# Optimization experiments

Hardware: AMD Instinct MI355X
Metric: run time of the kernel (lower is better)

## Reference

```python
import jax, jax.numpy as jnp
import numpy as np

B, G, D, E = 16, 2048, 2048, 32          # batch, genes, drug fp dim, gene embed dim
NL, NM, H, GS = 16, 4, 6, 64             # n leaves, n mids, term hidden, genes per leaf
GAMMA, NDRUG, EPS = 0.5, 1024, 1e-5

def _bn3(x):  # BatchNorm1d on [B, C, L], training stats, affine at init (gamma=1, beta=0)
    m = x.mean(axis=(0, 2), keepdims=True)
    v = x.var(axis=(0, 2), keepdims=True)
    return (x - m) / jnp.sqrt(v + EPS)

def _bn2(x):  # BatchNorm1d on [B, C]
    m = x.mean(axis=0, keepdims=True)
    v = x.var(axis=0, keepdims=True)
    return (x - m) / jnp.sqrt(v + EPS)

def _term(ci, W1, b1, Wc, bc, Wd, bd):
    # ci: [B, E, in] child input; returns ([B,H,E] 3d out, [B,H] 2d out)
    h = jnp.einsum('bei,hi->bhe', ci, W1) + b1[None, :, None]      # linear -> permute
    h = _bn3(h)
    c = jnp.einsum('bhe,kh->bke', h, Wc) + bc[None, :, None]       # context layer
    out3d = _bn3(c)                                                # [B,H,E]
    mean = out3d.mean(axis=1)                                      # [B,E]
    out2d = _bn2(jnp.tanh(mean @ Wd.T + bd))                       # dimension layer
    return out3d, out2d

def setup_inputs():
    key = jax.random.key(0)
    ks = iter(jax.random.split(key, 64))
    def rn(shape):
        return jax.random.normal(next(ks), shape, dtype=jnp.float32) * 0.05
    x = jax.random.normal(next(ks), (B, G + D + 1), dtype=jnp.float32)
    idx = jax.random.randint(next(ks), (B,), 0, NDRUG)
    x = x.at[:, -1].set(idx.astype(jnp.float32))
    table = jax.random.randint(next(ks), (NDRUG, G), 0, G, dtype=jnp.int32)
    inp = dict(x=x, table=table,
        W_rbf=rn((E, G)), b_rbf=rn((E,)), emb=rn((G, E)),
        W_dg=rn((NL, GS, G)), b_dg=rn((NL, GS)),
        Wl1=rn((NL, H, GS)), bl1=rn((NL, H)), Wlc=rn((NL, H, H)), blc=rn((NL, H)),
        Wld=rn((NL, H, E)), bld=rn((NL, H)),
        Wm1=rn((NM, H, 4 * H)), bm1=rn((NM, H)), Wmc=rn((NM, H, H)), bmc=rn((NM, H)),
        Wmd=rn((NM, H, E)), bmd=rn((NM, H)),
        Wr1=rn((H, 4 * H)), br1=rn((H,)), Wrc=rn((H, H)), brc=rn((H,)),
        Wrd=rn((H, E)), brd=rn((H,)),
        Wd1=rn((100, D)), bd1=rn((100,)), Wd2=rn((50, 100)), bd2=rn((50,)),
        Wd3=rn((H, 50)), bd3=rn((H,)),
        Wf=rn((6, 2 * H)), bf=rn((6,)), Wfa=rn((1, 6)), bfa=rn((1,)),
        Wfo=rn((1, 1)), bfo=rn((1,)))
    return inp

def reference(x, W_rbf, b_rbf, emb, W_dg, b_dg,
              Wl1, bl1, Wlc, blc, Wld, bld,
              Wm1, bm1, Wmc, bmc, Wmd, bmd,
              Wr1, br1, Wrc, brc, Wrd, brd,
              Wd1, bd1, Wd2, bd2, Wd3, bd3,
              Wf, bf, Wfa, bfa, Wfo, bfo, table):
    g = x[:, :G]
    drug = x[:, G:G + D]
    idx = x[:, G + D].astype(jnp.int32)
    # RBF kernel: [B, G, G]
    vect = jnp.exp(-GAMMA * jnp.square(g[:, :, None] - g[:, None, :]))
    gv = jnp.einsum('bij,ej->bie', vect, W_rbf) + b_rbf            # [B,G,E]
    lv = emb[table[idx]]                                            # [B,G,E]
    gf = (gv + lv).transpose(0, 2, 1)                               # [B,E,G]
    # per-leaf direct gene layers
    gene_out = jnp.einsum('beg,lkg->lbek', gf, W_dg) + b_dg[:, None, None, :]  # [NL,B,E,GS]
    leaf3d, _ = jax.vmap(_term)(gene_out, Wl1, bl1, Wlc, blc, Wld, bld)        # [NL,B,H,E]
    # mid terms: concat 4 leaf children along feature dim
    a = leaf3d.transpose(0, 1, 3, 2).reshape(NM, 4, B, E, H)
    a = jnp.moveaxis(a, 1, 3).reshape(NM, B, E, 4 * H)
    mid3d, _ = jax.vmap(_term)(a, Wm1, bm1, Wmc, bmc, Wmd, bmd)                # [NM,B,H,E]
    r = jnp.moveaxis(mid3d.transpose(0, 1, 3, 2), 0, 2).reshape(B, E, 4 * H)
    _, root2d = _term(r, Wr1, br1, Wrc, brc, Wrd, brd)                          # [B,H]
    # drug MLP
    d = drug
    for Wl, bl in ((Wd1, bd1), (Wd2, bd2), (Wd3, bd3)):
        d = _bn2(jnp.tanh(d @ Wl.T + bl))
    fin = jnp.concatenate([root2d, d], axis=1)                                  # [B,2H]
    out = _bn2(jnp.tanh(fin @ Wf.T + bf))
    aux = jnp.tanh(out @ Wfa.T + bfa)
    return aux @ Wfo.T + bfo                                                    # [B,1]
```

## Files before the change

### kernel.cpp

```cpp
#include <hip/hip_runtime.h>
#include <hip/hip_bf16.h>

#define Bb 16
#define Gg 2048
#define Dd 2048
#define XS 4097
#define EPSf 1e-5f
#define CEXP (-0.72134752044448170368f)

typedef unsigned int u32;
typedef __attribute__((ext_vector_type(8))) short bf16x8;
typedef __attribute__((ext_vector_type(4))) float f32x4;

union U16 { uint4 u; bf16x8 v; };

__device__ inline float fast_exp2(float x) {
#if __has_builtin(__builtin_amdgcn_exp2f)
  return __builtin_amdgcn_exp2f(x);
#else
  return exp2f(x);
#endif
}

__device__ inline u32 pk2(float a, float b) {
// ... 18 lines not shown
__device__ inline float wred(float v) {
  #pragma unroll
  for (int o = 32; o > 0; o >>= 1) v += __shfl_xor(v, o, 64);
  return v;
}

__global__ __launch_bounds__(256) void k_split(const float* __restrict__ Wrbf,
                                               const float* __restrict__ Wdg,
                                               u32* __restrict__ Rhi, u32* __restrict__ Rlo,
                                               u32* __restrict__ Dhi, u32* __restrict__ Dlo) {
  int c = blockIdx.x * 256 + threadIdx.x;
  const float* src;
  u32 *dhi, *dlo;
  if (c < 8192) {
    int h = c >> 12, ks = (c >> 6) & 63, l = c & 63;
    src = Wrbf + (h * 16 + (l & 15)) * Gg + ks * 32 + (l >> 4) * 8;
    dhi = Rhi + (size_t)c * 4; dlo = Rlo + (size_t)c * 4;
  } else {
    int cc = c - 8192;
    int nf = cc >> 12, ks = (cc >> 6) & 63, l = cc & 63;
    src = Wdg + (size_t)(nf * 16 + (l & 15)) * Gg + ks * 32 + (l >> 4) * 8;
    dhi = Dhi + (size_t)cc * 4; dlo = Dlo + (size_t)cc * 4;
  }
  float4 f0 = *(const float4*)src;
  float4 f1 = *(const float4*)(src + 4);
  float f[8] = {f0.x, f0.y, f0.z, f0.w, f1.x, f1.y, f1.z, f1.w};
  U16 hi, lo;
  split8(f, hi, lo);
  *(uint4*)dhi = hi.u;
  *(uint4*)dlo = lo.u;
}

__global__ __launch_bounds__(512) void k_rbf(const float* __restrict__ x,
                                             const u32* __restrict__ Whi,
                                             const u32* __restrict__ Wlo,
                                             const int* __restrict__ table,
                                             const float* __restrict__ emb,
                                             const float* __restrict__ brbf,
                                             u32* __restrict__ Ahi,
                                             u32* __restrict__ Alo) {
  __shared__ float g_s[2048];
  __shared__ u32 w_s[8192];
  const int tid = threadIdx.x;
  const int lane = tid & 63, wid = tid >> 6;
  const int b = blockIdx.y;
  const int i0w = blockIdx.x * 128 + wid * 16;
  #pragma unroll
  for (int q = 0; q < 4; ++q) g_s[tid * 4 + q] = x[(size_t)b * XS + tid * 4 + q];
  const float gi = x[(size_t)b * XS + i0w + (lane & 15)];
  f32x4 acc0 = {0.f, 0.f, 0.f, 0.f};
  f32x4 acc1 = {0.f, 0.f, 0.f, 0.f};
  const int jb = (lane >> 4) * 8;

  for (int chunk = 0; chunk < 8; ++chunk) {
    __syncthreads();
    #pragma unroll
    for (int sg = 0; sg < 4; ++sg) {
      int seg = wid * 4 + sg;
      int arr = seg >> 4, h = (seg >> 3) & 1, ksl = seg & 7;
      const u32* src = (arr ? Wlo : Whi) +
          (((size_t)h * 64 + chunk * 8 + ksl) * 64 + lane) * 4;
      *(uint4*)&w_s[seg * 256 + lane * 4] = *(const uint4*)src;
    }
    __syncthreads();
    #pragma unroll
    for (int ksl = 0; ksl < 8; ++ksl) {
      const float* gp = &g_s[chunk * 256 + ksl * 32 + jb];
      float4 gja = *(const float4*)gp;
      float4 gjb = *(const float4*)(gp + 4);
      float gv[8] = {gja.x, gja.y, gja.z, gja.w, gjb.x, gjb.y, gjb.z, gjb.w};
      float kv[8];
      #pragma unroll
      for (int q = 0; q < 8; ++q) {
        float d = gi - gv[q];
        kv[q] = fast_exp2(d * d * CEXP);
      }
      U16 ah, al;
      split8(kv, ah, al);
      U16 w0h, w1h, w0l, w1l;
      w0h.u = *(const uint4*)&w_s[(ksl) * 256 + lane * 4];
      w1h.u = *(const uint4*)&w_s[(8 + ksl) * 256 + lane * 4];
      w0l.u = *(const uint4*)&w_s[(16 + ksl) * 256 + lane * 4];
      w1l.u = *(const uint4*)&w_s[(24 + ksl) * 256 + lane * 4];
      acc0 = __builtin_amdgcn_mfma_f32_16x16x32_bf16(ah.v, w0h.v, acc0, 0, 0, 0);
      acc0 = __builtin_amdgcn_mfma_f32_16x16x32_bf16(al.v, w0h.v, acc0, 0, 0, 0);
      acc0 = __builtin_amdgcn_mfma_f32_16x16x32_bf16(ah.v, w0l.v, acc0, 0, 0, 0);
      acc1 = __builtin_amdgcn_mfma_f32_16x16x32_bf16(ah.v, w1h.v, acc1, 0, 0, 0);
      acc1 = __builtin_amdgcn_mfma_f32_16x16x32_bf16(al.v, w1h.v, acc1, 0, 0, 0);
      acc1 = __builtin_amdgcn_mfma_f32_16x16x32_bf16(ah.v, w1l.v, acc1, 0, 0, 0);
    }
  }
  const int idx = (int)x[(size_t)b * XS + Gg + Dd];
  const int eloc = lane & 15, quad = lane >> 4;
  const int ks = i0w >> 5;
  const int lp = (2 * ((i0w >> 4) & 1) + (quad >> 1)) * 16 + eloc;
  const int hs = quad & 1;
  #pragma unroll
  for (int hb = 0; hb < 2; ++hb) {
    const int e = hb * 16 + eloc;
    const float bias = brbf[e];
    f32x4 a = hb ? acc1 : acc0;
    float v[4];
    #pragma unroll
    for (int r = 0; r < 4; ++r) {
      int i = i0w + quad * 4 + r;
      int t = table[idx * Gg + i];
      v[r] = a[r] + bias + emb[t * 32 + e];
    }
    size_t off = ((size_t)((b * 2 + hb) * 64 + ks) * 64 + lp) * 4 + hs * 2;
    Ahi[off]     = pk2(v[0], v[1]);
    Ahi[off + 1] = pk2(v[2], v[3]);
    Alo[off]     = pk2(v[0] - bftrunc(v[0]), v[1] - bftrunc(v[1]));
    Alo[off + 1] = pk2(v[2] - bftrunc(v[2]), v[3] - bftrunc(v[3]));
  }
}

__global__ __launch_bounds__(256) void k_mm(const u32* __restrict__ Ahi,
                                            const u32* __restrict__ Alo,
                                            const u32* __restrict__ Bhi,
                                            const u32* __restrict__ Blo,
                                            float* __restrict__ part) {
  __shared__ u32 s_mm[6144];
  const int tid = threadIdx.x;
  const int lane = tid & 63, wid = tid >> 6;
  const int id = blockIdx.x;
  const int pl = id & 7, by = (id >> 3) & 7, ph = id >> 6;
  const int p = ph * 8 + pl;
  const int bx = p >> 2, kc = p & 3;
  const int wm = wid >> 1, wn = wid & 1;
  f32x4 acc[2][4];
  #pragma unroll
  for (int mf = 0; mf < 2; ++mf)
    #pragma unroll
    for (int nf = 0; nf < 4; ++nf) acc[mf][nf] = (f32x4){0.f, 0.f, 0.f, 0.f};

  for (int stage = 0; stage < 16; ++stage) {
    const int ks = kc * 16 + stage;
    __syncthreads();
    #pragma unroll
    for (int q = 0; q < 6; ++q) {
      int seg = wid * 6 + q;
      const u32* src;
      if (seg < 8) {
        int hl = seg >> 2, mf = seg & 3;
        src = (hl ? Alo : Ahi) + (((size_t)(by * 4 + mf) * 64 + ks) * 64 + lane) * 4;
      } else {
        int t = seg - 8, hl = t >> 3, nf = t & 7;
        src = (hl ? Blo : Bhi) + (((size_t)(bx * 8 + nf) * 64 + ks) * 64 + lane) * 4;
      }
      *(uint4*)&s_mm[seg * 256 + lane * 4] = *(const uint4*)src;
    }
    __syncthreads();
    U16 ah[2], al[2], bh[4], bl[4];
    #pragma unroll
    for (int mf = 0; mf < 2; ++mf) {
      ah[mf].u = *(const uint4*)&s_mm[(0 + wm * 2 + mf) * 256 + lane * 4];
      al[mf].u = *(const uint4*)&s_mm[(4 + wm * 2 + mf) * 256 + lane * 4];
    }
    #pragma unroll
    for (int nf = 0; nf < 4; ++nf) {
      bh[nf].u = *(const uint4*)&s_mm[(8 + wn * 4 + nf) * 256 + lane * 4];
      bl[nf].u = *(const uint4*)&s_mm[(16 + wn * 4 + nf) * 256 + lane * 4];
    }
    #pragma unroll
    for (int mf = 0; mf < 2; ++mf) {
      #pragma unroll
      for (int nf = 0; nf < 4; ++nf) {
        acc[mf][nf] = __builtin_amdgcn_mfma_f32_16x16x32_bf16(ah[mf].v, bh[nf].v, acc[mf][nf], 0, 0, 0);
        acc[mf][nf] = __builtin_amdgcn_mfma_f32_16x16x32_bf16(al[mf].v, bh[nf].v, acc[mf][nf], 0, 0, 0);
        acc[mf][nf] = __builtin_amdgcn_mfma_f32_16x16x32_bf16(ah[mf].v, bl[nf].v, acc[mf][nf], 0, 0, 0);
      }
    }
  }
  const int quad = lane >> 4, nl = lane & 15;
  #pragma unroll
  for (int mf = 0; mf < 2; ++mf) {
    #pragma unroll
    for (int nf = 0; nf < 4; ++nf) {
      int n  = bx * 128 + wn * 64 + nf * 16 + nl;
      int m0 = by * 64 + wm * 32 + mf * 16 + quad * 4;
      float4 st = make_float4(acc[mf][nf][0], acc[mf][nf][1], acc[mf][nf][2], acc[mf][nf][3]);
      *(float4*)&part[(size_t)kc * 524288 + (size_t)n * 512 + m0] = st;
    }
  }
}

__device__ inline void bn512(float* v, int wv, int lane,
                             float (*r1)[6], float (*r2)[6]) {
  float s[6], q[6];
  #pragma unroll
  for (int c = 0; c < 6; ++c) {
    float a = v[c];
    s[c] = wred(a);
    q[c] = wred(a * a);
  }
  __syncthreads();
  if (lane == 0) {
    #pragma unroll
    for (int c = 0; c < 6; ++c) { r1[wv][c] = s[c]; r2[wv][c] = q[c]; }
  }
  __syncthreads();
  #pragma unroll
  for (int c = 0; c < 6; ++c) {
    float S = 0.f, Q = 0.f;
    #pragma unroll
    for (int w = 0; w < 8; ++w) { S += r1[w][c]; Q += r2[w][c]; }
    float m  = S * (1.0f / 512.0f);
    float va = Q * (1.0f / 512.0f) - m * m;
    v[c] = (v[c] - m) * rsqrtf(va + EPSf);
  }
}

__global__ __launch_bounds__(512) void k_leaf(const float* __restrict__ part,
                                              const float* __restrict__ bdg,
                                              const float* __restrict__ W1,
                                              const float* __restrict__ b1,
                                              const float* __restrict__ Wc,
                                              const float* __restrict__ bc,
                                              float* __restrict__ outp) {
  const int l = blockIdx.x, tid = threadIdx.x;
  const int wv = tid >> 6, lane = tid & 63;
  __shared__ float r1[8][6], r2[8][6];
  float cv[64];
  #pragma unroll
  for (int i = 0; i < 64; ++i) {
    int n = l * 64 + i;
    const float* pp = part + (size_t)n * 512 + tid;
    cv[i] = pp[0] + pp[524288] + pp[2 * 524288] + pp[3 * 524288] + bdg[n];
  }
  const float* w1 = W1 + l * 6 * 64;
  float h[6];
  #pragma unroll
  for (int hh = 0; hh < 6; ++hh) {
    float s = b1[l * 6 + hh];
    #pragma unroll
    for (int i = 0; i < 64; ++i) s = fmaf(cv[i], w1[hh * 64 + i], s);
    h[hh] = s;
  }
  bn512(h, wv, lane, r1, r2);
  float c[6];
  #pragma unroll
  for (int k = 0; k < 6; ++k) {
    float s = bc[l * 6 + k];
    #pragma unroll
    for (int hh = 0; hh < 6; ++hh) s = fmaf(h[hh], Wc[l * 36 + k * 6 + hh], s);
    c[k] = s;
  }
  bn512(c, wv, lane, r1, r2);
  float* o = outp + (((size_t)(l >> 2) * 512 + tid) * 24 + (l & 3) * 6);
  #pragma unroll
  for (int k = 0; k < 6; ++k) o[k] = c[k];
}

__global__ __launch_bounds__(512) void k_mid(const float* __restrict__ gin,
                                             const float* __restrict__ W1,
                                             const float* __restrict__ b1,
                                             const float* __restrict__ Wc,
                                             const float* __restrict__ bc,
                                             float* __restrict__ outp) {
  const int l = blockIdx.x, tid = threadIdx.x;
  const int wv = tid >> 6, lane = tid & 63;
  __shared__ float r1[8][6], r2[8][6];
  const float* ci = gin + ((size_t)l * 512 + tid) * 24;
  float cv[24];
  #pragma unroll
  for (int q = 0; q < 6; ++q) *(float4*)&cv[q * 4] = ((const float4*)ci)[q];
  const float* w1 = W1 + l * 6 * 24;
  float h[6];
  #pragma unroll
  for (int hh = 0; hh < 6; ++hh) {
    float s = b1[l * 6 + hh];
    #pragma unroll
    for (int i = 0; i < 24; ++i) s = fmaf(cv[i], w1[hh * 24 + i], s);
    h[hh] = s;
  }
  bn512(h, wv, lane, r1, r2);
  float c[6];
  #pragma unroll
  for (int k = 0; k < 6; ++k) {
    float s = bc[l * 6 + k];
    #pragma unroll
    for (int hh = 0; hh < 6; ++hh) s = fmaf(h[hh], Wc[l * 36 + k * 6 + hh], s);
    c[k] = s;
  }
  bn512(c, wv, lane, r1, r2);
  float* o = outp + ((size_t)tid * 24 + l * 6);
  #pragma unroll
  for (int k = 0; k < 6; ++k) o[k] = c[k];
}

__global__ __launch_bounds__(512) void k_root(const float* __restrict__ rootin,
                                              const float* __restrict__ Wr1,
                                              const float* __restrict__ br1,
                                              const float* __restrict__ Wrc,
                                              const float* __restrict__ brc,
                                              const float* __restrict__ Wrd,
                                              const float* __restrict__ brd,
                                              float* __restrict__ r2d) {
  const int tid = threadIdx.x;
  const int wv = tid >> 6, lane = tid & 63;
  __shared__ float r1[8][6], r2[8][6];
  const float* ci = rootin + (size_t)tid * 24;
  float cv[24];
  #pragma unroll
  for (int q = 0; q < 6; ++q) *(float4*)&cv[q * 4] = ((const float4*)ci)[q];
  float h[6];
  #pragma unroll
  for (int hh = 0; hh < 6; ++hh) {
    float s = br1[hh];
    #pragma unroll
    for (int i = 0; i < 24; ++i) s = fmaf(cv[i], Wr1[hh * 24 + i], s);
    h[hh] = s;
  }
  bn512(h, wv, lane, r1, r2);
  float c[6];
  #pragma unroll
  for (int k = 0; k < 6; ++k) {
    float s = brc[k];
    #pragma unroll
    for (int hh = 0; hh < 6; ++hh) s = fmaf(h[hh], Wrc[k * 6 + hh], s);
    c[k] = s;
  }
  bn512(c, wv, lane, r1, r2);
  float mv = (c[0] + c[1] + c[2] + c[3] + c[4] + c[5]) * (1.0f / 6.0f);
  __shared__ float shm[512];
  shm[tid] = mv;
  __syncthreads();
  __shared__ float st[96];
  if (tid < 96) {
    int b = tid / 6, hh = tid % 6;
    float s = brd[hh];
    #pragma unroll
    for (int e = 0; e < 32; ++e) s = fmaf(shm[b * 32 + e], Wrd[hh * 32 + e], s);
    st[tid] = tanhf(s);
  }
  __syncthreads();
  if (tid < 6) {
    float S = 0.f, Q = 0.f;
    for (int b = 0; b < 16; ++b) { float v = st[b * 6 + tid]; S += v; Q += v * v; }
    float m = S * (1.0f / 16.0f), va = Q * (1.0f / 16.0f) - m * m;
    float iv = rsqrtf(va + EPSf);
    for (int b = 0; b < 16; ++b) r2d[b * 6 + tid] = (st[b * 6 + tid] - m) * iv;
  }
}

__global__ __launch_bounds__(1024) void k_drug1(const float* __restrict__ x,
                                                const float* __restrict__ Wd1,
                                                const float* __restrict__ bd1,
                                                float* __restrict__ d1) {
  const int c = blockIdx.x;
  const int tid = threadIdx.x;
  const int b = tid >> 6, lane = tid & 63;
  const float* xb = x + (size_t)b * XS + Gg;
  const float* w = Wd1 + (size_t)c * 2048;
  float s = 0.f;
  #pragma unroll
  for (int q = 0; q < 8; ++q) {
    int k = q * 256 + lane * 4;
    float4 xv = *(const float4*)(xb + k);
    float4 wv = *(const float4*)(w + k);
    s = fmaf(xv.x, wv.x, s);
    s = fmaf(xv.y, wv.y, s);
    s = fmaf(xv.z, wv.z, s);
    s = fmaf(xv.w, wv.w, s);
  }
  s = wred(s);
  __shared__ float y[16];
  if (lane == 0) y[b] = tanhf(s + bd1[c]);
  __syncthreads();
  if (tid < 16) {
    float S = 0.f, Q = 0.f;
    #pragma unroll
    for (int bb = 0; bb < 16; ++bb) { float v = y[bb]; S += v; Q += v * v; }
    float m = S * (1.0f / 16.0f), va = Q * (1.0f / 16.0f) - m * m;
    d1[tid * 100 + c] = (y[tid] - m) * rsqrtf(va + EPSf);
  }
}

__global__ __launch_bounds__(512) void k_final(const float* __restrict__ d1,
                                               const float* __restrict__ r2d,
                                               const float* __restrict__ Wd2,
                                               const float* __restrict__ bd2,
                                               const float* __restrict__ Wd3,
                                               const float* __restrict__ bd3,
                                               const float* __restrict__ Wf,
                                               const float* __restrict__ bf,
                                               const float* __restrict__ Wfa,
                                               const float* __restrict__ bfa,
                                               const float* __restrict__ Wfo,
                                               const float* __restrict__ bfo,
                                               float* __restrict__ out) {
  const int tid = threadIdx.x;
  __shared__ float s2[800], mu2[50], iv2[50];
  for (int u = tid; u < 800; u += 512) {
    int b = u / 50, c = u % 50;
    float s = bd2[c];
    for (int k = 0; k < 100; ++k) s = fmaf(d1[b * 100 + k], Wd2[c * 100 + k], s);
    s2[u] = tanhf(s);
  }
  __syncthreads();
  if (tid < 50) {
    float S = 0.f, Q = 0.f;
    #pragma unroll
    for (int b = 0; b < 16; ++b) { float v = s2[b * 50 + tid]; S += v; Q += v * v; }
    float m = S * (1.0f / 16.0f), va = Q * (1.0f / 16.0f) - m * m;
    mu2[tid] = m; iv2[tid] = rsqrtf(va + EPSf);
  }
  __syncthreads();
  __shared__ float s3[96], mu3[6], iv3[6];
  if (tid < 96) {
    int b = tid / 6, c = tid % 6;
    float s = bd3[c];
    for (int k = 0; k < 50; ++k)
      s = fmaf((s2[b * 50 + k] - mu2[k]) * iv2[k], Wd3[c * 50 + k], s);
    s3[tid] = tanhf(s);
  }
  __syncthreads();
  if (tid < 6) {
    float S = 0.f, Q = 0.f;
    #pragma unroll
    for (int b = 0; b < 16; ++b) { float v = s3[b * 6 + tid]; S += v; Q += v * v; }
    float m = S * (1.0f / 16.0f), va = Q * (1.0f / 16.0f) - m * m;
    mu3[tid] = m; iv3[tid] = rsqrtf(va + EPSf);
  }
  __syncthreads();
  __shared__ float sf[96], muf[6], ivf[6];
  if (tid < 96) {
    int b = tid / 6, c = tid % 6;
    float s = bf[c];
    #pragma unroll
    for (int q = 0; q < 6; ++q) s = fmaf(r2d[b * 6 + q], Wf[c * 12 + q], s);
    #pragma unroll
    for (int q = 0; q < 6; ++q)
      s = fmaf((s3[b * 6 + q] - mu3[q]) * iv3[q], Wf[c * 12 + 6 + q], s);
    sf[tid] = tanhf(s);
  }
  __syncthreads();
  if (tid < 6) {
    float S = 0.f, Q = 0.f;
    #pragma unroll
    for (int b = 0; b < 16; ++b) { float v = sf[b * 6 + tid]; S += v; Q += v * v; }
    float m = S * (1.0f / 16.0f), va = Q * (1.0f / 16.0f) - m * m;
    muf[tid] = m; ivf[tid] = rsqrtf(va + EPSf);
  }
  __syncthreads();
  if (tid < 16) {
    float s = bfa[0];
    #pragma unroll
    for (int q = 0; q < 6; ++q)
      s = fmaf((sf[tid * 6 + q] - muf[q]) * ivf[q], Wfa[q], s);
    float a = tanhf(s);
    out[tid] = a * Wfo[0] + bfo[0];
  }
}

extern "C" void kernel_launch(void* const* d_in, const int* in_sizes, int n_in,
                              void* d_out, int out_size, void* d_ws, size_t ws_size,
                              hipStream_t stream) {
  const float* x     = (const float*)d_in[0];
  const int*   table = (const int*)d_in[1];
  const float* Wrbf  = (const float*)d_in[2];
  const float* brbf  = (const float*)d_in[3];
  const float* emb   = (const float*)d_in[4];
  const float* Wdg   = (const float*)d_in[5];
  const float* bdg   = (const float*)d_in[6];
  const float* Wl1   = (const float*)d_in[7];
  const float* bl1   = (const float*)d_in[8];
  const float* Wlc   = (const float*)d_in[9];
  const float* blc   = (const float*)d_in[10];
  const float* Wm1   = (const float*)d_in[13];
  const float* bm1   = (const float*)d_in[14];
  const float* Wmc   = (const float*)d_in[15];
  const float* bmc   = (const float*)d_in[16];
  const float* Wr1   = (const float*)d_in[19];
  const float* br1   = (const float*)d_in[20];
  const float* Wrc   = (const float*)d_in[21];
  const float* brc   = (const float*)d_in[22];
  const float* Wrd   = (const float*)d_in[23];
  const float* brd   = (const float*)d_in[24];
  const float* Wd1   = (const float*)d_in[25];
  const float* bd1   = (const float*)d_in[26];
  const float* Wd2   = (const float*)d_in[27];
  const float* bd2   = (const float*)d_in[28];
  const float* Wd3   = (const float*)d_in[29];
  const float* bd3   = (const float*)d_in[30];
  const float* Wf    = (const float*)d_in[31];
  const float* bf    = (const float*)d_in[32];
  const float* Wfa   = (const float*)d_in[33];
  const float* bfa   = (const float*)d_in[34];
  const float* Wfo   = (const float*)d_in[35];
  const float* bfo   = (const float*)d_in[36];
  float* out = (float*)d_out;

  u32* Rhi = (u32*)d_ws;
  u32* Rlo = Rhi + 32768;
  u32* Dhi = Rlo + 32768;
  u32* Dlo = Dhi + 1048576;
  u32* Ahi = Dlo + 1048576;
  u32* Alo = Ahi + 524288;
  float* partB = (float*)(Alo + 524288);
  float* midin = partB + 4 * 524288;
  float* rootin= midin + 49152;
  float* r2d   = rootin + 12288;
  float* d1    = r2d + 96;

  hipLaunchKernelGGL(k_split, dim3(1056),   dim3(256),  0, stream, Wrbf, Wdg, Rhi, Rlo, Dhi, Dlo);
  hipLaunchKernelGGL(k_rbf,   dim3(16, 16), dim3(512),  0, stream, x, Rhi, Rlo, table, emb, brbf, Ahi, Alo);
  hipLaunchKernelGGL(k_mm,    dim3(256),    dim3(256),  0, stream, Ahi, Alo, Dhi, Dlo, partB);
  hipLaunchKernelGGL(k_leaf,  dim3(16),     dim3(512),  0, stream, partB, bdg, Wl1, bl1, Wlc, blc, midin);
  hipLaunchKernelGGL(k_mid,   dim3(4),      dim3(512),  0, stream, midin, Wm1, bm1, Wmc, bmc, rootin);
  hipLaunchKernelGGL(k_root,  dim3(1),      dim3(512),  0, stream, rootin, Wr1, br1, Wrc, brc, Wrd, brd, r2d);
  hipLaunchKernelGGL(k_drug1, dim3(100),    dim3(1024), 0, stream, x, Wd1, bd1, d1);
  hipLaunchKernelGGL(k_final, dim3(1),      dim3(512),  0, stream, d1, r2d, Wd2, bd2, Wd3, bd3,
                     Wf, bf, Wfa, bfa, Wfo, bfo, out);
}
```

Before: 125.0 us.

## Prefetch weight tiles, widen matmul blocks, split reduction kernel, fuse tail kernels

k_rbf and k_mm now load the next K-stage of weights into registers while the current stage is processed, so global loads overlap compute. k_mm goes to 512 threads with a 2x4 warp grid, so each warp holds fewer accumulators. A new k_gout kernel does the split-K reduction plus bias with coalesced float4 accesses; previously k_leaf did it using only 16 blocks. The mid, root and final kernels are merged into one 1024-thread k_tail kernel that keeps root inputs in shared memory, and k_drug1 is launched first. The trade-offs are higher register pressure and one extra pass over the partial buffer through global memory.

```diff
diff --git a/kernel.cpp b/kernel.cpp
--- a/kernel.cpp
+++ b/kernel.cpp
@@ -94,15 +94,27 @@
   f32x4 acc1 = {0.f, 0.f, 0.f, 0.f};
   const int jb = (lane >> 4) * 8;
 
+  uint4 pf[4];
+  #pragma unroll
+  for (int sg = 0; sg < 4; ++sg) {
+    int seg = wid * 4 + sg;
+    int arr = seg >> 4, h = (seg >> 3) & 1, ksl = seg & 7;
+    pf[sg] = *(const uint4*)((arr ? Wlo : Whi) +
+             (((size_t)h * 64 + 0 * 8 + ksl) * 64 + lane) * 4);
+  }
   for (int chunk = 0; chunk < 8; ++chunk) {
     __syncthreads();
     #pragma unroll
-    for (int sg = 0; sg < 4; ++sg) {
-      int seg = wid * 4 + sg;
-      int arr = seg >> 4, h = (seg >> 3) & 1, ksl = seg & 7;
-      const u32* src = (arr ? Wlo : Whi) +
-          (((size_t)h * 64 + chunk * 8 + ksl) * 64 + lane) * 4;
-      *(uint4*)&w_s[seg * 256 + lane * 4] = *(const uint4*)src;
+    for (int sg = 0; sg < 4; ++sg)
+      *(uint4*)&w_s[(wid * 4 + sg) * 256 + lane * 4] = pf[sg];
+    if (chunk < 7) {
+      #pragma unroll
+      for (int sg = 0; sg < 4; ++sg) {
+        int seg = wid * 4 + sg;
+        int arr = seg >> 4, h = (seg >> 3) & 1, ksl = seg & 7;
+        pf[sg] = *(const uint4*)((arr ? Wlo : Whi) +
+                 (((size_t)h * 64 + (chunk + 1) * 8 + ksl) * 64 + lane) * 4);
+      }
     }
     __syncthreads();
     #pragma unroll
@@ -157,7 +169,7 @@
   }
 }
 
-__global__ __launch_bounds__(256) void k_mm(const u32* __restrict__ Ahi,
+__global__ __launch_bounds__(512) void k_mm(const u32* __restrict__ Ahi,
                                             const u32* __restrict__ Alo,
                                             const u32* __restrict__ Bhi,
                                             const u32* __restrict__ Blo,
@@ -169,45 +181,64 @@
   const int pl = id & 7, by = (id >> 3) & 7, ph = id >> 6;
   const int p = ph * 8 + pl;
   const int bx = p >> 2, kc = p & 3;
-  const int wm = wid >> 1, wn = wid & 1;
-  f32x4 acc[2][4];
+  const int wm = wid >> 2, wn = wid & 3;
+  f32x4 acc[2][2];
   #pragma unroll
   for (int mf = 0; mf < 2; ++mf)
     #pragma unroll
-    for (int nf = 0; nf < 4; ++nf) acc[mf][nf] = (f32x4){0.f, 0.f, 0.f, 0.f};
-
+    for (int nf = 0; nf < 2; ++nf) acc[mf][nf] = (f32x4){0.f, 0.f, 0.f, 0.f};
+
+  uint4 pf[3];
+  #pragma unroll
+  for (int q = 0; q < 3; ++q) {
+    int seg = wid * 3 + q;
+    const u32* src;
+    if (seg < 8) {
+      int hl = seg >> 2, mf = seg & 3;
+      src = (hl ? Alo : Ahi) + (((size_t)(by * 4 + mf) * 64 + kc * 16) * 64 + lane) * 4;
+    } else {
+      int t = seg - 8, hl = t >> 3, nf = t & 7;
+      src = (hl ? Blo : Bhi) + (((size_t)(bx * 8 + nf) * 64 + kc * 16) * 64 + lane) * 4;
+    }
+    pf[q] = *(const uint4*)src;
+  }
   for (int stage = 0; stage < 16; ++stage) {
-    const int ks = kc * 16 + stage;
-    __syncthreads();
-    #pragma unroll
-    for (int q = 0; q < 6; ++q) {
-      int seg = wid * 6 + q;
-      const u32* src;
-      if (seg < 8) {
-        int hl = seg >> 2, mf = seg & 3;
-        src = (hl ? Alo : Ahi) + (((size_t)(by * 4 + mf) * 64 + ks) * 64 + lane) * 4;
-      } else {
-        int t = seg - 8, hl = t >> 3, nf = t & 7;
-        src = (hl ? Blo : Bhi) + (((size_t)(bx * 8 + nf) * 64 + ks) * 64 + lane) * 4;
+    __syncthreads();
+    #pragma unroll
+    for (int q = 0; q < 3; ++q)
+      *(uint4*)&s_mm[(wid * 3 + q) * 256 + lane * 4] = pf[q];
+    if (stage < 15) {
+      const int ks = kc * 16 + stage + 1;
+      #pragma unroll
+      for (int q = 0; q < 3; ++q) {
+        int seg = wid * 3 + q;
+        const u32* src;
+        if (seg < 8) {
+          int hl = seg >> 2, mf = seg & 3;
+          src = (hl ? Alo : Ahi) + (((size_t)(by * 4 + mf) * 64 + ks) * 64 + lane) * 4;
+        } else {
+          int t = seg - 8, hl = t >> 3, nf = t & 7;
+          src = (hl ? Blo : Bhi) + (((size_t)(bx * 8 + nf) * 64 + ks) * 64 + lane) * 4;
+        }
+        pf[q] = *(const uint4*)src;
       }
-      *(uint4*)&s_mm[seg * 256 + lane * 4] = *(const uint4*)src;
-    }
-    __syncthreads();
-    U16 ah[2], al[2], bh[4], bl[4];
+    }
+    __syncthreads();
+    U16 ah[2], al[2], bh[2], bl[2];
     #pragma unroll
     for (int mf = 0; mf < 2; ++mf) {
       ah[mf].u = *(const uint4*)&s_mm[(0 + wm * 2 + mf) * 256 + lane * 4];
       al[mf].u = *(const uint4*)&s_mm[(4 + wm * 2 + mf) * 256 + lane * 4];
     }
     #pragma unroll
-    for (int nf = 0; nf < 4; ++nf) {
-      bh[nf].u = *(const uint4*)&s_mm[(8 + wn * 4 + nf) * 256 + lane * 4];
-      bl[nf].u = *(const uint4*)&s_mm[(16 + wn * 4 + nf) * 256 + lane * 4];
+    for (int nf = 0; nf < 2; ++nf) {
+      bh[nf].u = *(const uint4*)&s_mm[(8 + wn * 2 + nf) * 256 + lane * 4];
+      bl[nf].u = *(const uint4*)&s_mm[(16 + wn * 2 + nf) * 256 + lane * 4];
     }
     #pragma unroll
     for (int mf = 0; mf < 2; ++mf) {
       #pragma unroll
-      for (int nf = 0; nf < 4; ++nf) {
+      for (int nf = 0; nf < 2; ++nf) {
         acc[mf][nf] = __builtin_amdgcn_mfma_f32_16x16x32_bf16(ah[mf].v, bh[nf].v, acc[mf][nf], 0, 0, 0);
         acc[mf][nf] = __builtin_amdgcn_mfma_f32_16x16x32_bf16(al[mf].v, bh[nf].v, acc[mf][nf], 0, 0, 0);
         acc[mf][nf] = __builtin_amdgcn_mfma_f32_16x16x32_bf16(ah[mf].v, bl[nf].v, acc[mf][nf], 0, 0, 0);
@@ -218,13 +249,29 @@
   #pragma unroll
   for (int mf = 0; mf < 2; ++mf) {
     #pragma unroll
-    for (int nf = 0; nf < 4; ++nf) {
-      int n  = bx * 128 + wn * 64 + nf * 16 + nl;
+    for (int nf = 0; nf < 2; ++nf) {
+      int n  = bx * 128 + wn * 32 + nf * 16 + nl;
       int m0 = by * 64 + wm * 32 + mf * 16 + quad * 4;
       float4 st = make_float4(acc[mf][nf][0], acc[mf][nf][1], acc[mf][nf][2], acc[mf][nf][3]);
       *(float4*)&part[(size_t)kc * 524288 + (size_t)n * 512 + m0] = st;
     }
   }
+}
+
+__global__ __launch_bounds__(256) void k_gout(const float4* __restrict__ part4,
+                                              const float* __restrict__ bdg,
+                                              float4* __restrict__ gout4) {
+  int f4 = blockIdx.x * 256 + threadIdx.x;
+  int n = f4 >> 7;
+  float4 a = part4[f4];
+  float4 b = part4[131072 + f4];
+  float4 c = part4[262144 + f4];
+  float4 d = part4[393216 + f4];
+  float bias = bdg[n];
+  gout4[f4] = make_float4(a.x + b.x + c.x + d.x + bias,
+                          a.y + b.y + c.y + d.y + bias,
+                          a.z + b.z + c.z + d.z + bias,
+                          a.w + b.w + c.w + d.w + bias);
 }
 
 __device__ inline void bn512(float* v, int wv, int lane,
@@ -253,8 +300,33 @@
   }
 }
 
-__global__ __launch_bounds__(512) void k_leaf(const float* __restrict__ part,
-                                              const float* __restrict__ bdg,
+__device__ inline void bn512g(float* v, int wv, int wbase, int lane,
+                              float (*r1)[6], float (*r2)[6]) {
+  float s[6], q[6];
+  #pragma unroll
+  for (int c = 0; c < 6; ++c) {
+    float a = v[c];
+    s[c] = wred(a);
+    q[c] = wred(a * a);
+  }
+  __syncthreads();
+  if (lane == 0) {
+    #pragma unroll
+    for (int c = 0; c < 6; ++c) { r1[wv][c] = s[c]; r2[wv][c] = q[c]; }
+  }
+  __syncthreads();
+  #pragma unroll
+  for (int c = 0; c < 6; ++c) {
+    float S = 0.f, Q = 0.f;
+    #pragma unroll
+    for (int w = 0; w < 8; ++w) { S += r1[wbase + w][c]; Q += r2[wbase + w][c]; }
+    float m  = S * (1.0f / 512.0f);
+    float va = Q * (1.0f / 512.0f) - m * m;
+    v[c] = (v[c] - m) * rsqrtf(va + EPSf);
+  }
+}
+
+__global__ __launch_bounds__(512) void k_leaf(const float* __restrict__ gout,
                                               const float* __restrict__ W1,
                                               const float* __restrict__ b1,
                                               const float* __restrict__ Wc,
@@ -265,11 +337,8 @@
   __shared__ float r1[8][6], r2[8][6];
   float cv[64];
   #pragma unroll
-  for (int i = 0; i < 64; ++i) {
-    int n = l * 64 + i;
-    const float* pp = part + (size_t)n * 512 + tid;
-    cv[i] = pp[0] + pp[524288] + pp[2 * 524288] + pp[3 * 524288] + bdg[n];
-  }
+  for (int i = 0; i < 64; ++i)
+    cv[i] = gout[(size_t)(l * 64 + i) * 512 + tid];
   const float* w1 = W1 + l * 6 * 64;
   float h[6];
   #pragma unroll
@@ -292,98 +361,6 @@
   float* o = outp + (((size_t)(l >> 2) * 512 + tid) * 24 + (l & 3) * 6);
   #pragma unroll
   for (int k = 0; k < 6; ++k) o[k] = c[k];
-}
-
-__global__ __launch_bounds__(512) void k_mid(const float* __restrict__ gin,
-                                             const float* __restrict__ W1,
-                                             const float* __restrict__ b1,
-                                             const float* __restrict__ Wc,
-                                             const float* __restrict__ bc,
-                                             float* __restrict__ outp) {
-  const int l = blockIdx.x, tid = threadIdx.x;
-  const int wv = tid >> 6, lane = tid & 63;
-  __shared__ float r1[8][6], r2[8][6];
-  const float* ci = gin + ((size_t)l * 512 + tid) * 24;
-  float cv[24];
-  #pragma unroll
-  for (int q = 0; q < 6; ++q) *(float4*)&cv[q * 4] = ((const float4*)ci)[q];
-  const float* w1 = W1 + l * 6 * 24;
-  float h[6];
-  #pragma unroll
-  for (int hh = 0; hh < 6; ++hh) {
-    float s = b1[l * 6 + hh];
-    #pragma unroll
-    for (int i = 0; i < 24; ++i) s = fmaf(cv[i], w1[hh * 24 + i], s);
-    h[hh] = s;
-  }
-  bn512(h, wv, lane, r1, r2);
-  float c[6];
-  #pragma unroll
-  for (int k = 0; k < 6; ++k) {
-    float s = bc[l * 6 + k];
-    #pragma unroll
-    for (int hh = 0; hh < 6; ++hh) s = fmaf(h[hh], Wc[l * 36 + k * 6 + hh], s);
-    c[k] = s;
-  }
-  bn512(c, wv, lane, r1, r2);
-  float* o = outp + ((size_t)tid * 24 + l * 6);
-  #pragma unroll
-  for (int k = 0; k < 6; ++k) o[k] = c[k];
-}
-
-__global__ __launch_bounds__(512) void k_root(const float* __restrict__ rootin,
-                                              const float* __restrict__ Wr1,
-                                              const float* __restrict__ br1,
-                                              const float* __restrict__ Wrc,
-                                              const float* __restrict__ brc,
-                                              const float* __restrict__ Wrd,
-                                              const float* __restrict__ brd,
-                                              float* __restrict__ r2d) {
-  const int tid = threadIdx.x;
-  const int wv = tid >> 6, lane = tid & 63;
-  __shared__ float r1[8][6], r2[8][6];
-  const float* ci = rootin + (size_t)tid * 24;
-  float cv[24];
-  #pragma unroll
-  for (int q = 0; q < 6; ++q) *(float4*)&cv[q * 4] = ((const float4*)ci)[q];
-  float h[6];
-  #pragma unroll
-  for (int hh = 0; hh < 6; ++hh) {
-    float s = br1[hh];
-    #pragma unroll
-    for (int i = 0; i < 24; ++i) s = fmaf(cv[i], Wr1[hh * 24 + i], s);
-    h[hh] = s;
-  }
-  bn512(h, wv, lane, r1, r2);
-  float c[6];
-  #pragma unroll
-  for (int k = 0; k < 6; ++k) {
-    float s = brc[k];
-    #pragma unroll
-    for (int hh = 0; hh < 6; ++hh) s = fmaf(h[hh], Wrc[k * 6 + hh], s);
-    c[k] = s;
-  }
-  bn512(c, wv, lane, r1, r2);
-  float mv = (c[0] + c[1] + c[2] + c[3] + c[4] + c[5]) * (1.0f / 6.0f);
-  __shared__ float shm[512];
-  shm[tid] = mv;
-  __syncthreads();
-  __shared__ float st[96];
-  if (tid < 96) {
-    int b = tid / 6, hh = tid % 6;
-    float s = brd[hh];
-    #pragma unroll
-    for (int e = 0; e < 32; ++e) s = fmaf(shm[b * 32 + e], Wrd[hh * 32 + e], s);
-    st[tid] = tanhf(s);
-  }
-  __syncthreads();
-  if (tid < 6) {
-    float S = 0.f, Q = 0.f;
-    for (int b = 0; b < 16; ++b) { float v = st[b * 6 + tid]; S += v; Q += v * v; }
-    float m = S * (1.0f / 16.0f), va = Q * (1.0f / 16.0f) - m * m;
-    float iv = rsqrtf(va + EPSf);
-    for (int b = 0; b < 16; ++b) r2d[b * 6 + tid] = (st[b * 6 + tid] - m) * iv;
-  }
 }
 
 __global__ __launch_bounds__(1024) void k_drug1(const float* __restrict__ x,
@@ -419,80 +396,162 @@
   }
 }
 
-__global__ __launch_bounds__(512) void k_final(const float* __restrict__ d1,
-                                               const float* __restrict__ r2d,
-                                               const float* __restrict__ Wd2,
-                                               const float* __restrict__ bd2,
-                                               const float* __restrict__ Wd3,
-                                               const float* __restrict__ bd3,
-                                               const float* __restrict__ Wf,
-                                               const float* __restrict__ bf,
-                                               const float* __restrict__ Wfa,
-                                               const float* __restrict__ bfa,
-                                               const float* __restrict__ Wfo,
-                                               const float* __restrict__ bfo,
+__global__ __launch_bounds__(1024) void k_tail(const float* __restrict__ midin,
+                                               const float* __restrict__ d1,
+                                               const float* __restrict__ Wm1, const float* __restrict__ bm1,
+                                               const float* __restrict__ Wmc, const float* __restrict__ bmc,
+                                               const float* __restrict__ Wr1, const float* __restrict__ br1,
+                                               const float* __restrict__ Wrc, const float* __restrict__ brc,
+                                               const float* __restrict__ Wrd, const float* __restrict__ brd,
+                                               const float* __restrict__ Wd2, const float* __restrict__ bd2,
+                                               const float* __restrict__ Wd3, const float* __restrict__ bd3,
+                                               const float* __restrict__ Wf,  const float* __restrict__ bf,
+                                               const float* __restrict__ Wfa, const float* __restrict__ bfa,
+                                               const float* __restrict__ Wfo, const float* __restrict__ bfo,
                                                float* __restrict__ out) {
   const int tid = threadIdx.x;
-  __shared__ float s2[800], mu2[50], iv2[50];
-  for (int u = tid; u < 800; u += 512) {
-    int b = u / 50, c = u % 50;
-    float s = bd2[c];
-    for (int k = 0; k < 100; ++k) s = fmaf(d1[b * 100 + k], Wd2[c * 100 + k], s);
-    s2[u] = tanhf(s);
+  const int wv = tid >> 6, lane = tid & 63;
+  const int half = tid >> 9, t512 = tid & 511;
+  const int wbase = half * 8;
+  __shared__ float r1[16][6], r2[16][6];
+  __shared__ float rin[512 * 24];
+
+  for (int lp = 0; lp < 2; ++lp) {
+    const int l = lp * 2 + half;
+    const float* ci = midin + ((size_t)l * 512 + t512) * 24;
+    float cv[24];
+    #pragma unroll
+    for (int q = 0; q < 6; ++q) *(float4*)&cv[q * 4] = ((const float4*)ci)[q];
+    const float* w1 = Wm1 + l * 144;
+    float h[6];
+    #pragma unroll
+    for (int hh = 0; hh < 6; ++hh) {
+      float s = bm1[l * 6 + hh];
+      #pragma unroll
+      for (int i = 0; i < 24; ++i) s = fmaf(cv[i], w1[hh * 24 + i], s);
+      h[hh] = s;
+    }
+    bn512g(h, wv, wbase, lane, r1, r2);
+    float c[6];
+    #pragma unroll
+    for (int k = 0; k < 6; ++k) {
+      float s = bmc[l * 6 + k];
+      #pragma unroll
+      for (int hh = 0; hh < 6; ++hh) s = fmaf(h[hh], Wmc[l * 36 + k * 6 + hh], s);
+      c[k] = s;
+    }
+    bn512g(c, wv, wbase, lane, r1, r2);
+    #pragma unroll
+    for (int k = 0; k < 6; ++k) rin[t512 * 24 + l * 6 + k] = c[k];
   }
   __syncthreads();
-  if (tid < 50) {
-    float S = 0.f, Q = 0.f;
-    #pragma unroll
-    for (int b = 0; b < 16; ++b) { float v = s2[b * 50 + tid]; S += v; Q += v * v; }
-    float m = S * (1.0f / 16.0f), va = Q * (1.0f / 16.0f) - m * m;
-    mu2[tid] = m; iv2[tid] = rsqrtf(va + EPSf);
-  }
-  __syncthreads();
-  __shared__ float s3[96], mu3[6], iv3[6];
-  if (tid < 96) {
-    int b = tid / 6, c = tid % 6;
-    float s = bd3[c];
-    for (int k = 0; k < 50; ++k)
-      s = fmaf((s2[b * 50 + k] - mu2[k]) * iv2[k], Wd3[c * 50 + k], s);
-    s3[tid] = tanhf(s);
-  }
-  __syncthreads();
-  if (tid < 6) {
-    float S = 0.f, Q = 0.f;
-    #pragma unroll
-    for (int b = 0; b < 16; ++b) { float v = s3[b * 6 + tid]; S += v; Q += v * v; }
-    float m = S * (1.0f / 16.0f), va = Q * (1.0f / 16.0f) - m * m;
-    mu3[tid] = m; iv3[tid] = rsqrtf(va + EPSf);
-  }
-  __syncthreads();
-  __shared__ float sf[96], muf[6], ivf[6];
-  if (tid < 96) {
-    int b = tid / 6, c = tid % 6;
-    float s = bf[c];
-    #pragma unroll
-    for (int q = 0; q < 6; ++q) s = fmaf(r2d[b * 6 + q], Wf[c * 12 + q], s);
-    #pragma unroll
-    for (int q = 0; q < 6; ++q)
-      s = fmaf((s3[b * 6 + q] - mu3[q]) * iv3[q], Wf[c * 12 + 6 + q], s);
-    sf[tid] = tanhf(s);
-  }
-  __syncthreads();
-  if (tid < 6) {
-    float S = 0.f, Q = 0.f;
-    #pragma unroll
-    for (int b = 0; b < 16; ++b) { float v = sf[b * 6 + tid]; S += v; Q += v * v; }
-    float m = S * (1.0f / 16.0f), va = Q * (1.0f / 16.0f) - m * m;
-    muf[tid] = m; ivf[tid] = rsqrtf(va + EPSf);
-  }
-  __syncthreads();
-  if (tid < 16) {
-    float s = bfa[0];
-    #pragma unroll
-    for (int q = 0; q < 6; ++q)
-      s = fmaf((sf[tid * 6 + q] - muf[q]) * ivf[q], Wfa[q], s);
-    float a = tanhf(s);
-    out[tid] = a * Wfo[0] + bfo[0];
+
+  {
+    float cv[24];
+    #pragma unroll
+    for (int q = 0; q < 24; ++q) cv[q] = rin[t512 * 24 + q];
+    float h[6];
+    #pragma unroll
+    for (int hh = 0; hh < 6; ++hh) {
+      float s = br1[hh];
+      #pragma unroll
+      for (int i = 0; i < 24; ++i) s = fmaf(cv[i], Wr1[hh * 24 + i], s);
+      h[hh] = s;
+    }
+    bn512g(h, wv, wbase, lane, r1, r2);
+    float c[6];
+    #pragma unroll
+    for (int k = 0; k < 6; ++k) {
+      float s = brc[k];
+      #pragma unroll
+      for (int hh = 0; hh < 6; ++hh) s = fmaf(h[hh], Wrc[k * 6 + hh], s);
+      c[k] = s;
+    }
+    bn512g(c, wv, wbase, lane, r1, r2);
+    float mv = (c[0] + c[1] + c[2] + c[3] + c[4] + c[5]) * (1.0f / 6.0f);
+    __shared__ float shm[512];
+    if (half == 0) shm[t512] = mv;
+    __syncthreads();
+    __shared__ float st[96];
+    if (tid < 96) {
+      int b = tid / 6, hh = tid % 6;
+      float s = brd[hh];
+      #pragma unroll
+      for (int e = 0; e < 32; ++e) s = fmaf(shm[b * 32 + e], Wrd[hh * 32 + e], s);
+      st[tid] = tanhf(s);
+    }
+    __syncthreads();
+    __shared__ float r2d[96];
+    if (tid < 6) {
+      float S = 0.f, Q = 0.f;
+      for (int b = 0; b < 16; ++b) { float v = st[b * 6 + tid]; S += v; Q += v * v; }
+      float m = S * (1.0f / 16.0f), va = Q * (1.0f / 16.0f) - m * m;
+      float iv = rsqrtf(va + EPSf);
+      for (int b = 0; b < 16; ++b) r2d[b * 6 + tid] = (st[b * 6 + tid] - m) * iv;
+    }
+    __syncthreads();
+
+    __shared__ float s2[800], mu2[50], iv2[50];
+    if (tid < 800) {
+      int b = tid / 50, cc = tid % 50;
+      float s = bd2[cc];
+      for (int k = 0; k < 100; ++k) s = fmaf(d1[b * 100 + k], Wd2[cc * 100 + k], s);
+      s2[tid] = tanhf(s);
+    }
+    __syncthreads();
+    if (tid < 50) {
+      float S = 0.f, Q = 0.f;
+      #pragma unroll
+      for (int b = 0; b < 16; ++b) { float v = s2[b * 50 + tid]; S += v; Q += v * v; }
+      float m = S * (1.0f / 16.0f), va = Q * (1.0f / 16.0f) - m * m;
+      mu2[tid] = m; iv2[tid] = rsqrtf(va + EPSf);
+    }
+    __syncthreads();
+    __shared__ float s3[96], mu3[6], iv3[6];
+    if (tid < 96) {
+      int b = tid / 6, cc = tid % 6;
+      float s = bd3[cc];
+      for (int k = 0; k < 50; ++k)
+        s = fmaf((s2[b * 50 + k] - mu2[k]) * iv2[k], Wd3[cc * 50 + k], s);
+      s3[tid] = tanhf(s);
+    }
+    __syncthreads();
+    if (tid < 6) {
+      float S = 0.f, Q = 0.f;
+      #pragma unroll
+      for (int b = 0; b < 16; ++b) { float v = s3[b * 6 + tid]; S += v; Q += v * v; }
+      float m = S * (1.0f / 16.0f), va = Q * (1.0f / 16.0f) - m * m;
+      mu3[tid] = m; iv3[tid] = rsqrtf(va + EPSf);
+    }
+    __syncthreads();
+    __shared__ float sf[96], muf[6], ivf[6];
+    if (tid < 96) {
+      int b = tid / 6, cc = tid % 6;
+      float s = bf[cc];
+      #pragma unroll
+      for (int q = 0; q < 6; ++q) s = fmaf(r2d[b * 6 + q], Wf[cc * 12 + q], s);
+      #pragma unroll
+      for (int q = 0; q < 6; ++q)
+        s = fmaf((s3[b * 6 + q] - mu3[q]) * iv3[q], Wf[cc * 12 + 6 + q], s);
+      sf[tid] = tanhf(s);
+    }
+    __syncthreads();
+    if (tid < 6) {
+      float S = 0.f, Q = 0.f;
+      #pragma unroll
+      for (int b = 0; b < 16; ++b) { float v = sf[b * 6 + tid]; S += v; Q += v * v; }
+      float m = S * (1.0f / 16.0f), va = Q * (1.0f / 16.0f) - m * m;
+      muf[tid] = m; ivf[tid] = rsqrtf(va + EPSf);
+    }
+    __syncthreads();
+    if (tid < 16) {
+      float s = bfa[0];
+      #pragma unroll
+      for (int q = 0; q < 6; ++q)
+        s = fmaf((sf[tid * 6 + q] - muf[q]) * ivf[q], Wfa[q], s);
+      float a = tanhf(s);
+      out[tid] = a * Wfo[0] + bfo[0];
+    }
   }
 }
 
@@ -541,18 +600,17 @@
   u32* Ahi = Dlo + 1048576;
   u32* Alo = Ahi + 524288;
   float* partB = (float*)(Alo + 524288);
-  float* midin = partB + 4 * 524288;
-  float* rootin= midin + 49152;
-  float* r2d   = rootin + 12288;
-  float* d1    = r2d + 96;
-
+  float* gout  = partB + 4 * 524288;
+  float* midin = gout + 524288;
+  float* d1    = midin + 49152;
+
+  hipLaunchKernelGGL(k_drug1, dim3(100),    dim3(1024), 0, stream, x, Wd1, bd1, d1);
   hipLaunchKernelGGL(k_split, dim3(1056),   dim3(256),  0, stream, Wrbf, Wdg, Rhi, Rlo, Dhi, Dlo);
   hipLaunchKernelGGL(k_rbf,   dim3(16, 16), dim3(512),  0, stream, x, Rhi, Rlo, table, emb, brbf, Ahi, Alo);
-  hipLaunchKernelGGL(k_mm,    dim3(256),    dim3(256),  0, stream, Ahi, Alo, Dhi, Dlo, partB);
-  hipLaunchKernelGGL(k_leaf,  dim3(16),     dim3(512),  0, stream, partB, bdg, Wl1, bl1, Wlc, blc, midin);
-  hipLaunchKernelGGL(k_mid,   dim3(4),      dim3(512),  0, stream, midin, Wm1, bm1, Wmc, bmc, rootin);
-  hipLaunchKernelGGL(k_root,  dim3(1),      dim3(512),  0, stream, rootin, Wr1, br1, Wrc, brc, Wrd, brd, r2d);
-  hipLaunchKernelGGL(k_drug1, dim3(100),    dim3(1024), 0, stream, x, Wd1, bd1, d1);
-  hipLaunchKernelGGL(k_final, dim3(1),      dim3(512),  0, stream, d1, r2d, Wd2, bd2, Wd3, bd3,
-                     Wf, bf, Wfa, bfa, Wfo, bfo, out);
-}
+  hipLaunchKernelGGL(k_mm,    dim3(256),    dim3(512),  0, stream, Ahi, Alo, Dhi, Dlo, partB);
+  hipLaunchKernelGGL(k_gout,  dim3(512),    dim3(256),  0, stream, (const float4*)partB, bdg, (float4*)gout);
+  hipLaunchKernelGGL(k_leaf,  dim3(16),     dim3(512),  0, stream, gout, Wl1, bl1, Wlc, blc, midin);
+  hipLaunchKernelGGL(k_tail,  dim3(1),      dim3(1024), 0, stream, midin, d1,
+                     Wm1, bm1, Wmc, bmc, Wr1, br1, Wrc, brc, Wrd, brd,
+                     Wd2, bd2, Wd3, bd3, Wf, bf, Wfa, bfa, Wfo, bfo, out);
+}
```

Result: slower. 149.6 us (+19.6%).

## Prefetch global tiles into registers, widen k_mm blocks, split partial reduction kernel

Applied to the files above, without the earlier changes.

k_rbf and k_mm now load the next stage's global tiles into registers while the current stage is computed, a simple software pipeline meant to hide global load latency. k_mm moves to 512 threads with a smaller per-wave output tile (2x2 fragments) to raise wave count. A new k_gout kernel sums the four split-K partials plus bias with wide parallelism, instead of k_leaf doing it over only 16 blocks. k_final stages Wd2 and d1 in padded shared memory and unrolls its loops, and k_drug1 is launched first. These add a kernel launch and extra global traffic for the gout buffer in exchange for better latency hiding and parallelism.

```diff
diff --git a/kernel.cpp b/kernel.cpp
--- a/kernel.cpp
+++ b/kernel.cpp
@@ -94,15 +94,27 @@
   f32x4 acc1 = {0.f, 0.f, 0.f, 0.f};
   const int jb = (lane >> 4) * 8;
 
+  uint4 pf[4];
+  #pragma unroll
+  for (int sg = 0; sg < 4; ++sg) {
+    int seg = wid * 4 + sg;
+    int arr = seg >> 4, h = (seg >> 3) & 1, ksl = seg & 7;
+    pf[sg] = *(const uint4*)((arr ? Wlo : Whi) +
+             (((size_t)h * 64 + 0 * 8 + ksl) * 64 + lane) * 4);
+  }
   for (int chunk = 0; chunk < 8; ++chunk) {
     __syncthreads();
     #pragma unroll
-    for (int sg = 0; sg < 4; ++sg) {
-      int seg = wid * 4 + sg;
-      int arr = seg >> 4, h = (seg >> 3) & 1, ksl = seg & 7;
-      const u32* src = (arr ? Wlo : Whi) +
-          (((size_t)h * 64 + chunk * 8 + ksl) * 64 + lane) * 4;
-      *(uint4*)&w_s[seg * 256 + lane * 4] = *(const uint4*)src;
+    for (int sg = 0; sg < 4; ++sg)
+      *(uint4*)&w_s[(wid * 4 + sg) * 256 + lane * 4] = pf[sg];
+    if (chunk < 7) {
+      #pragma unroll
+      for (int sg = 0; sg < 4; ++sg) {
+        int seg = wid * 4 + sg;
+        int arr = seg >> 4, h = (seg >> 3) & 1, ksl = seg & 7;
+        pf[sg] = *(const uint4*)((arr ? Wlo : Whi) +
+                 (((size_t)h * 64 + (chunk + 1) * 8 + ksl) * 64 + lane) * 4);
+      }
     }
     __syncthreads();
     #pragma unroll
@@ -157,7 +169,7 @@
   }
 }
 
-__global__ __launch_bounds__(256) void k_mm(const u32* __restrict__ Ahi,
+__global__ __launch_bounds__(512) void k_mm(const u32* __restrict__ Ahi,
                                             const u32* __restrict__ Alo,
                                             const u32* __restrict__ Bhi,
                                             const u32* __restrict__ Blo,
@@ -169,45 +181,64 @@
   const int pl = id & 7, by = (id >> 3) & 7, ph = id >> 6;
   const int p = ph * 8 + pl;
   const int bx = p >> 2, kc = p & 3;
-  const int wm = wid >> 1, wn = wid & 1;
-  f32x4 acc[2][4];
+  const int wm = wid >> 2, wn = wid & 3;
+  f32x4 acc[2][2];
   #pragma unroll
   for (int mf = 0; mf < 2; ++mf)
     #pragma unroll
-    for (int nf = 0; nf < 4; ++nf) acc[mf][nf] = (f32x4){0.f, 0.f, 0.f, 0.f};
-
+    for (int nf = 0; nf < 2; ++nf) acc[mf][nf] = (f32x4){0.f, 0.f, 0.f, 0.f};
+
+  uint4 pf[3];
+  #pragma unroll
+  for (int q = 0; q < 3; ++q) {
+    int seg = wid * 3 + q;
+    const u32* src;
+    if (seg < 8) {
+      int hl = seg >> 2, mf = seg & 3;
+      src = (hl ? Alo : Ahi) + (((size_t)(by * 4 + mf) * 64 + kc * 16) * 64 + lane) * 4;
+    } else {
+      int t = seg - 8, hl = t >> 3, nf = t & 7;
+      src = (hl ? Blo : Bhi) + (((size_t)(bx * 8 + nf) * 64 + kc * 16) * 64 + lane) * 4;
+    }
+    pf[q] = *(const uint4*)src;
+  }
   for (int stage = 0; stage < 16; ++stage) {
-    const int ks = kc * 16 + stage;
     __syncthreads();
     #pragma unroll
-    for (int q = 0; q < 6; ++q) {
-      int seg = wid * 6 + q;
-      const u32* src;
-      if (seg < 8) {
-        int hl = seg >> 2, mf = seg & 3;
-        src = (hl ? Alo : Ahi) + (((size_t)(by * 4 + mf) * 64 + ks) * 64 + lane) * 4;
-      } else {
-        int t = seg - 8, hl = t >> 3, nf = t & 7;
-        src = (hl ? Blo : Bhi) + (((size_t)(bx * 8 + nf) * 64 + ks) * 64 + lane) * 4;
+    for (int q = 0; q < 3; ++q)
+      *(uint4*)&s_mm[(wid * 3 + q) * 256 + lane * 4] = pf[q];
+    if (stage < 15) {
+      const int ks = kc * 16 + stage + 1;
+      #pragma unroll
+      for (int q = 0; q < 3; ++q) {
+        int seg = wid * 3 + q;
+        const u32* src;
+        if (seg < 8) {
+          int hl = seg >> 2, mf = seg & 3;
+          src = (hl ? Alo : Ahi) + (((size_t)(by * 4 + mf) * 64 + ks) * 64 + lane) * 4;
+        } else {
+          int t = seg - 8, hl = t >> 3, nf = t & 7;
+          src = (hl ? Blo : Bhi) + (((size_t)(bx * 8 + nf) * 64 + ks) * 64 + lane) * 4;
+        }
+        pf[q] = *(const uint4*)src;
       }
-      *(uint4*)&s_mm[seg * 256 + lane * 4] = *(const uint4*)src;
     }
     __syncthreads();
-    U16 ah[2], al[2], bh[4], bl[4];
+    U16 ah[2], al[2], bh[2], bl[2];
     #pragma unroll
     for (int mf = 0; mf < 2; ++mf) {
       ah[mf].u = *(const uint4*)&s_mm[(0 + wm * 2 + mf) * 256 + lane * 4];
       al[mf].u = *(const uint4*)&s_mm[(4 + wm * 2 + mf) * 256 + lane * 4];
     }
     #pragma unroll
-    for (int nf = 0; nf < 4; ++nf) {
-      bh[nf].u = *(const uint4*)&s_mm[(8 + wn * 4 + nf) * 256 + lane * 4];
-      bl[nf].u = *(const uint4*)&s_mm[(16 + wn * 4 + nf) * 256 + lane * 4];
+    for (int nf = 0; nf < 2; ++nf) {
+      bh[nf].u = *(const uint4*)&s_mm[(8 + wn * 2 + nf) * 256 + lane * 4];
+      bl[nf].u = *(const uint4*)&s_mm[(16 + wn * 2 + nf) * 256 + lane * 4];
     }
     #pragma unroll
     for (int mf = 0; mf < 2; ++mf) {
       #pragma unroll
-      for (int nf = 0; nf < 4; ++nf) {
+      for (int nf = 0; nf < 2; ++nf) {
         acc[mf][nf] = __builtin_amdgcn_mfma_f32_16x16x32_bf16(ah[mf].v, bh[nf].v, acc[mf][nf], 0, 0, 0);
         acc[mf][nf] = __builtin_amdgcn_mfma_f32_16x16x32_bf16(al[mf].v, bh[nf].v, acc[mf][nf], 0, 0, 0);
         acc[mf][nf] = __builtin_amdgcn_mfma_f32_16x16x32_bf16(ah[mf].v, bl[nf].v, acc[mf][nf], 0, 0, 0);
@@ -218,13 +249,29 @@
   #pragma unroll
   for (int mf = 0; mf < 2; ++mf) {
     #pragma unroll
-    for (int nf = 0; nf < 4; ++nf) {
-      int n  = bx * 128 + wn * 64 + nf * 16 + nl;
+    for (int nf = 0; nf < 2; ++nf) {
+      int n  = bx * 128 + wn * 32 + nf * 16 + nl;
       int m0 = by * 64 + wm * 32 + mf * 16 + quad * 4;
       float4 st = make_float4(acc[mf][nf][0], acc[mf][nf][1], acc[mf][nf][2], acc[mf][nf][3]);
       *(float4*)&part[(size_t)kc * 524288 + (size_t)n * 512 + m0] = st;
     }
   }
+}
+
+__global__ __launch_bounds__(256) void k_gout(const float4* __restrict__ part4,
+                                              const float* __restrict__ bdg,
+                                              float4* __restrict__ gout4) {
+  int f4 = blockIdx.x * 256 + threadIdx.x;
+  int n = f4 >> 7;
+  float4 a = part4[f4];
+  float4 b = part4[131072 + f4];
+  float4 c = part4[262144 + f4];
+  float4 d = part4[393216 + f4];
+  float bias = bdg[n];
+  gout4[f4] = make_float4(a.x + b.x + c.x + d.x + bias,
+                          a.y + b.y + c.y + d.y + bias,
+                          a.z + b.z + c.z + d.z + bias,
+                          a.w + b.w + c.w + d.w + bias);
 }
 
 __device__ inline void bn512(float* v, int wv, int lane,
@@ -253,8 +300,7 @@
   }
 }
 
-__global__ __launch_bounds__(512) void k_leaf(const float* __restrict__ part,
-                                              const float* __restrict__ bdg,
+__global__ __launch_bounds__(512) void k_leaf(const float* __restrict__ gout,
                                               const float* __restrict__ W1,
                                               const float* __restrict__ b1,
                                               const float* __restrict__ Wc,
@@ -265,11 +311,8 @@
   __shared__ float r1[8][6], r2[8][6];
   float cv[64];
   #pragma unroll
-  for (int i = 0; i < 64; ++i) {
-    int n = l * 64 + i;
-    const float* pp = part + (size_t)n * 512 + tid;
-    cv[i] = pp[0] + pp[524288] + pp[2 * 524288] + pp[3 * 524288] + bdg[n];
-  }
+  for (int i = 0; i < 64; ++i)
+    cv[i] = gout[(size_t)(l * 64 + i) * 512 + tid];
   const float* w1 = W1 + l * 6 * 64;
   float h[6];
   #pragma unroll
@@ -433,11 +476,17 @@
                                                const float* __restrict__ bfo,
                                                float* __restrict__ out) {
   const int tid = threadIdx.x;
+  __shared__ float w2s[50 * 101];
+  __shared__ float d1s[1600];
+  for (int u = tid; u < 5000; u += 512) w2s[(u / 100) * 101 + (u % 100)] = Wd2[u];
+  for (int u = tid; u < 1600; u += 512) d1s[u] = d1[u];
+  __syncthreads();
   __shared__ float s2[800], mu2[50], iv2[50];
   for (int u = tid; u < 800; u += 512) {
     int b = u / 50, c = u % 50;
     float s = bd2[c];
-    for (int k = 0; k < 100; ++k) s = fmaf(d1[b * 100 + k], Wd2[c * 100 + k], s);
+    #pragma unroll
+    for (int k = 0; k < 100; ++k) s = fmaf(d1s[b * 100 + k], w2s[c * 101 + k], s);
     s2[u] = tanhf(s);
   }
   __syncthreads();
@@ -453,6 +502,7 @@
   if (tid < 96) {
     int b = tid / 6, c = tid % 6;
     float s = bd3[c];
+    #pragma unroll
     for (int k = 0; k < 50; ++k)
       s = fmaf((s2[b * 50 + k] - mu2[k]) * iv2[k], Wd3[c * 50 + k], s);
     s3[tid] = tanhf(s);
@@ -541,18 +591,20 @@
   u32* Ahi = Dlo + 1048576;
   u32* Alo = Ahi + 524288;
   float* partB = (float*)(Alo + 524288);
-  float* midin = partB + 4 * 524288;
+  float* gout  = partB + 4 * 524288;
+  float* midin = gout + 524288;
   float* rootin= midin + 49152;
   float* r2d   = rootin + 12288;
   float* d1    = r2d + 96;
 
+  hipLaunchKernelGGL(k_drug1, dim3(100),    dim3(1024), 0, stream, x, Wd1, bd1, d1);
   hipLaunchKernelGGL(k_split, dim3(1056),   dim3(256),  0, stream, Wrbf, Wdg, Rhi, Rlo, Dhi, Dlo);
   hipLaunchKernelGGL(k_rbf,   dim3(16, 16), dim3(512),  0, stream, x, Rhi, Rlo, table, emb, brbf, Ahi, Alo);
-  hipLaunchKernelGGL(k_mm,    dim3(256),    dim3(256),  0, stream, Ahi, Alo, Dhi, Dlo, partB);
-  hipLaunchKernelGGL(k_leaf,  dim3(16),     dim3(512),  0, stream, partB, bdg, Wl1, bl1, Wlc, blc, midin);
+  hipLaunchKernelGGL(k_mm,    dim3(256),    dim3(512),  0, stream, Ahi, Alo, Dhi, Dlo, partB);
+  hipLaunchKernelGGL(k_gout,  dim3(512),    dim3(256),  0, stream, (const float4*)partB, bdg, (float4*)gout);
+  hipLaunchKernelGGL(k_leaf,  dim3(16),     dim3(512),  0, stream, gout, Wl1, bl1, Wlc, blc, midin);
   hipLaunchKernelGGL(k_mid,   dim3(4),      dim3(512),  0, stream, midin, Wm1, bm1, Wmc, bmc, rootin);
   hipLaunchKernelGGL(k_root,  dim3(1),      dim3(512),  0, stream, rootin, Wr1, br1, Wrc, brc, Wrd, brd, r2d);
-  hipLaunchKernelGGL(k_drug1, dim3(100),    dim3(1024), 0, stream, x, Wd1, bd1, d1);
   hipLaunchKernelGGL(k_final, dim3(1),      dim3(512),  0, stream, d1, r2d, Wd2, bd2, Wd3, bd3,
                      Wf, bf, Wfa, bfa, Wfo, bfo, out);
 }
```

Measured after the change: 128.7 us. 1.03x slower.
